# Kernel tuning notes

Measured on AMD Instinct MI355X. Metric: run time of the kernel, lower is better.

Reference implementation:

```python
import math
import jax, jax.numpy as jnp
import numpy as np

D = 1024
NH = 16
DH = D // NH


def setup_inputs() -> dict:
    key = jax.random.key(0)
    k1, k2, k3 = jax.random.split(key, 3)
    x = jax.random.normal(k1, (2, 2048, D), dtype=jnp.float32)
    s = 1.0 / math.sqrt(D)
    W_qkv = jax.random.normal(k2, (D, 3 * D), dtype=jnp.float32) * s
    W_o = jax.random.normal(k3, (D, D), dtype=jnp.float32) * s
    return {"x": x, "W_qkv": W_qkv, "W_o": W_o}


def _rope(q, k, base=10000.0):
    # q, k: [B, H, T, dh]
    half = q.shape[-1] // 2
    freqs = jnp.arange(half, dtype=q.dtype) / half
    theta = 1.0 / base ** freqs                      # [half]
    t = jnp.arange(q.shape[-2], dtype=q.dtype)       # [T]
    ang = t[:, None] * theta[None, :]                # [T, half]
    cos = jnp.cos(ang)[None, None, :, :]
    sin = jnp.sin(ang)[None, None, :, :]

    def rot(x):
        x1, x2 = x[..., :half], x[..., half:]
        return jnp.concatenate([x1 * cos - x2 * sin, x1 * sin + x2 * cos], axis=-1)

    return rot(q), rot(k)


def reference(x, W_qkv, W_o):
    B, T, d = x.shape
    qkv = x @ W_qkv                                   # [B, T, 3D]
    q, k, v = jnp.split(qkv, 3, axis=-1)
    q = q.reshape(B, T, NH, DH).transpose(0, 2, 1, 3)  # [B, H, T, dh]
    k = k.reshape(B, T, NH, DH).transpose(0, 2, 1, 3)
    v = v.reshape(B, T, NH, DH).transpose(0, 2, 1, 3)
    q, k = _rope(q, k)
    att = jnp.einsum('bhtd,bhsd->bhts', q, k) / math.sqrt(DH)  # [B, H, T, T]
    mask = jnp.triu(jnp.full((T, T), -jnp.inf, dtype=att.dtype), 1)
    att = att + mask
    w = jax.nn.softmax(att, axis=-1)
    y = jnp.einsum('bhts,bhsd->bhtd', w, v)           # [B, H, T, dh]
    y = y.transpose(0, 2, 1, 3).reshape(B, T, d)
    return y @ W_o
```

## Files before the change

### kernel.cpp

```cpp
#include <hip/hip_runtime.h>

typedef __bf16 bf16x8 __attribute__((ext_vector_type(8)));
typedef float f32x4 __attribute__((ext_vector_type(4)));
typedef float f32x16 __attribute__((ext_vector_type(16)));

constexpr int SEQ = 2048;
constexpr int DMODEL = 1024;

#define GLL(gp, lp)                                                              \
  __builtin_amdgcn_global_load_lds((const __attribute__((address_space(1))) void*)(gp), \
                                   (__attribute__((address_space(3))) void*)(lp), 16, 0, 0)

__global__ __launch_bounds__(256) void prep_kernel(const float* __restrict__ x,
                                                   const float* __restrict__ Wqkv,
                                                   const float* __restrict__ Wo,
                                                   __bf16* __restrict__ xbf,
                                                   __bf16* __restrict__ WqkvT,
                                                   __bf16* __restrict__ WoT,
                                                   float2* __restrict__ sct) {
  __shared__ __bf16 tile[64][72];
  int blk = blockIdx.x, t = threadIdx.x;

  if (blk < 256) {
    int i = blk * 256 + t;
    int tt = i >> 5, j = i & 31;
    float theta = exp2f(-(float)j * 0.41524101186092953f);
    float s, c;
    __sincosf((float)tt * theta, &s, &c);
    sct[i] = make_float2(c, s);
    return;
  }
  if (blk >= 1280) {
    size_t i = (size_t)(blk - 1280) * 256 + t;
    const float* sp = x + i * 8;
    float4 f0 = *reinterpret_cast<const float4*>(sp);
    float4 f1 = *reinterpret_cast<const float4*>(sp + 4);
    alignas(16) __bf16 tmp[8];
    tmp[0] = (__bf16)f0.x; tmp[1] = (__bf16)f0.y; tmp[2] = (__bf16)f0.z; tmp[3] = (__bf16)f0.w;
    tmp[4] = (__bf16)f1.x; tmp[5] = (__bf16)f1.y; tmp[6] = (__bf16)f1.z; tmp[7] = (__bf16)f1.w;
    *reinterpret_cast<uint4*>(xbf + i * 8) = *reinterpret_cast<const uint4*>(tmp);
    return;
  }
  const float* src;
  __bf16* dst;
  int C, R, c0, r0;
  if (blk < 512) {
    int idx = blk - 256;
    src = Wo; dst = WoT; R = 1024; C = 1024;
    c0 = (idx & 15) * 64; r0 = (idx >> 4) * 64;
  } else {
    int idx = blk - 512;
    src = Wqkv; dst = WqkvT; R = 1024; C = 3072;
    c0 = (idx % 48) * 64; r0 = (idx / 48) * 64;
  }
#pragma unroll
  for (int p = 0; p < 2; ++p) {
    int flat = p * 256 + t;
    int i = flat >> 3;
    int j8 = (flat & 7) * 8;
    const float* sp = &src[(size_t)(r0 + i) * C + c0 + j8];
    float4 f0 = *reinterpret_cast<const float4*>(sp);
    float4 f1 = *reinterpret_cast<const float4*>(sp + 4);
    tile[i][j8 + 0] = (__bf16)f0.x; tile[i][j8 + 1] = (__bf16)f0.y;
    tile[i][j8 + 2] = (__bf16)f0.z; tile[i][j8 + 3] = (__bf16)f0.w;
    tile[i][j8 + 4] = (__bf16)f1.x; tile[i][j8 + 5] = (__bf16)f1.y;
    tile[i][j8 + 6] = (__bf16)f1.z; tile[i][j8 + 7] = (__bf16)f1.w;
  }
  __syncthreads();
#pragma unroll
  for (int p = 0; p < 2; ++p) {
    int flat = p * 256 + t;
    int i = flat >> 3;
    int j8 = (flat & 7) * 8;
    alignas(16) __bf16 tmp[8];
#pragma unroll
    for (int jj = 0; jj < 8; ++jj) tmp[jj] = tile[j8 + jj][i];
    *reinterpret_cast<uint4*>(&dst[(size_t)(c0 + i) * R + r0 + j8]) =
        *reinterpret_cast<const uint4*>(tmp);
  }
}

template <typename CT, int BN, int MODE>
__global__ __launch_bounds__(256) void gemm_bt_lds(const __bf16* __restrict__ A,
                                                   const __bf16* __restrict__ BT,
                                                   CT* __restrict__ C,
                                                   int M, int N, int K, int lda, int ldc,
                                                   const float2* __restrict__ sct,
                                                   __bf16* __restrict__ vt) {
  constexpr int MF = (BN == 128) ? 4 : 2;
  __shared__ __align__(16) __bf16 A_lds[128][64];
  __shared__ __align__(16) __bf16 B_lds[BN][64];
  int tid = threadIdx.x;
  int lane = tid & 63, w = tid >> 6;
  int g = lane >> 4, l15 = lane & 15;
  int wr = (BN == 128) ? (w >> 1) : w;
  int wc = (BN == 128) ? (w & 1) : 0;
  int m0 = blockIdx.x * 128;
  int n0 = blockIdx.y * BN;
  int srow = lane >> 3, scol = (lane & 7) * 8;

  const __bf16* ag = A + (size_t)(m0 + w * 32 + srow) * lda + scol;
  const __bf16* bg = BT + (size_t)(n0 + w * (BN / 4) + srow) * K + scol;

  f32x4 acc[MF][4] = {};

  for (int k0 = 0; k0 < K; k0 += 64) {
    __syncthreads();
#pragma unroll
    for (int i = 0; i < 4; ++i)
      GLL(ag + (size_t)(i * 8) * lda + k0, &A_lds[w * 32 + i * 8][0]);
#pragma unroll
    for (int i = 0; i < BN / 32; ++i)
      GLL(bg + (size_t)(i * 8) * K + k0, &B_lds[w * (BN / 4) + i * 8][0]);
    __syncthreads();
#pragma unroll
    for (int kk = 0; kk < 2; ++kk) {
      bf16x8 a[MF], bb[4];
#pragma unroll
      for (int m = 0; m < MF; ++m)
        a[m] = *reinterpret_cast<const bf16x8*>(&A_lds[wr * (MF * 16) + m * 16 + l15][kk * 32 + g * 8]);
#pragma unroll
      for (int n = 0; n < 4; ++n)
        bb[n] = *reinterpret_cast<const bf16x8*>(&B_lds[wc * 64 + n * 16 + l15][kk * 32 + g * 8]);
#pragma unroll
      for (int m = 0; m < MF; ++m)
#pragma unroll
        for (int n = 0; n < 4; ++n)
          acc[m][n] = __builtin_amdgcn_mfma_f32_16x16x32_bf16(a[m], bb[n], acc[m][n], 0, 0, 0);
    }
  }

  if constexpr (MODE == 3) {
    if (n0 >= 2048) {
      __shared__ __bf16 T_lds[128][72];
      int b = m0 >> 11;
      int s_base = m0 & (SEQ - 1);
#pragma unroll
      for (int half = 0; half < 2; ++half) {
        __syncthreads();
        if (wc == half) {
#pragma unroll
          for (int m = 0; m < MF; ++m)
#pragma unroll
            for (int n = 0; n < 4; ++n)
#pragma unroll
              for (int r = 0; r < 4; ++r)
                T_lds[wr * 64 + m * 16 + 4 * g + r][n * 16 + l15] = (__bf16)acc[m][n][r];
        }
        __syncthreads();
        int head = ((n0 - 2048) >> 6) + half;
        int bh = b * 16 + head;
        int d = tid >> 2;
        int s8 = (tid & 3) * 32;
        __bf16* dst = vt + (size_t)bh * 64 * SEQ + (size_t)d * SEQ + s_base + s8;
#pragma unroll
        for (int j = 0; j < 4; ++j) {
          alignas(16) __bf16 tmp[8];
#pragma unroll
          for (int e = 0; e < 8; ++e) tmp[e] = T_lds[s8 + j * 8 + e][d];
          *reinterpret_cast<uint4*>(dst + j * 8) = *reinterpret_cast<const uint4*>(tmp);
        }
      }
      return;
    }
    bool isq = (n0 < 1024);
    float sc = isq ? 0.18033688011112042f : 1.0f;
#pragma unroll
    for (int m = 0; m < MF; ++m)
#pragma unroll
      for (int r = 0; r < 4; ++r) {
        int row = m0 + wr * (MF * 16) + m * 16 + 4 * g + r;
        int t = row & (SEQ - 1);
#pragma unroll
        for (int n = 0; n < 2; ++n) {
          int j = n * 16 + l15;
          float2 cs = sct[(t << 5) + j];
          float x1 = acc[m][n][r], x2 = acc[m][n + 2][r];
          acc[m][n][r]     = (x1 * cs.x - x2 * cs.y) * sc;
          acc[m][n + 2][r] = (x1 * cs.y + x2 * cs.x) * sc;
        }
      }
  }

#pragma unroll
  for (int m = 0; m < MF; ++m)
#pragma unroll
    for (int n = 0; n < 4; ++n)
#pragma unroll
      for (int r = 0; r < 4; ++r) {
        int row = m0 + wr * (MF * 16) + m * 16 + 4 * g + r;
        int col = n0 + wc * 64 + n * 16 + l15;
        C[(size_t)row * ldc + col] = (CT)acc[m][n][r];
      }
}

__device__ inline uint32_t pkbf(float a, float b) {
  union { __bf16 h[2]; uint32_t u; } z;
  z.h[0] = (__bf16)a; z.h[1] = (__bf16)b;
  return z.u;
}

__device__ inline __bf16* slot_base(int gi, __bf16* qkv, __bf16* xbf, int q_local) {
  if (gi < 1024)
    return qkv + (size_t)(gi * 4 + (q_local >> 4)) * 3072 + 2048 + (q_local & 15) * 64;
  return xbf + (size_t)(gi - 1024) * 4096 + (size_t)q_local * 64;
}

__global__ __launch_bounds__(128, 3) void attn_kernel(__bf16* __restrict__ qkv,
                                                      const __bf16* __restrict__ vt,
                                                      __bf16* __restrict__ xbf,
                                                      float* __restrict__ pml) {
  __shared__ __align__(16) __bf16 K_lds[2][64][64];

  int tid = threadIdx.x;
  int w = tid >> 6, lane = tid & 63;
  int l31 = lane & 31, hi = lane >> 5;
  int bid = blockIdx.x;
  int it = bid >> 5, bh = bid & 31;
  int b = bh >> 4, h = bh & 15;

  int qc = 31 - (it >> 1);
  int half = it & 1;
  int NTf = qc + 1;
  int hs = (NTf + 1) >> 1;
  int kv0 = half ? hs : 0;
  int kv1 = half ? NTf : hs;
  int NT = kv1 - kv0;

  __bf16* qbase = qkv + (size_t)b * SEQ * 3072 + h * 64;
  const __bf16* kbase = qbase + 1024;
  const __bf16* vtb = vt + (size_t)bh * 64 * SEQ;

  int q_g = qc * 64 + w * 32 + l31;

  int r8 = lane >> 3;
  int cxe = 8 * ((lane & 7) ^ r8);

  auto STAGE = [&](int bufv, int t) {
#pragma unroll
    for (int i = 0; i < 4; ++i) {
      int R = w * 32 + i * 8;
      GLL(kbase + (size_t)(t * 64 + R + r8) * 3072 + cxe, &K_lds[bufv][R][0]);
    }
  };

  bf16x8 qf[4];
#pragma unroll
  for (int ds = 0; ds < 4; ++ds)
    qf[ds] = *reinterpret_cast<const bf16x8*>(qbase + (size_t)q_g * 3072 + ds * 16 + 8 * hi);

  f32x16 oacc[2] = {};
  float l_run = 0.f;
  const float MFIX = 8.0f;

  if (NT > 0) STAGE(0, kv0);
  __syncthreads();

  int buf = 0;
  for (int jb = 0; jb < NT; ++jb) {
    int kt_g = kv0 + jb;
    bool pre = (jb + 1 < NT);
    if (pre) STAGE(buf ^ 1, kt_g + 1);

    uint4 vr[8];
#pragma unroll
    for (int dt = 0; dt < 2; ++dt)
#pragma unroll
      for (int ks = 0; ks < 4; ++ks)
        vr[dt * 4 + ks] = *reinterpret_cast<const uint4*>(
            vtb + (size_t)(dt * 32 + l31) * SEQ + kt_g * 64 + ks * 16 + 8 * hi);

    f32x16 sacc[2] = {};
    __builtin_amdgcn_s_setprio(1);
#pragma unroll
    for (int kt = 0; kt < 2; ++kt) {
#pragma unroll
      for (int ds = 0; ds < 4; ++ds) {
        bf16x8 kf = *reinterpret_cast<const bf16x8*>(
            &K_lds[buf][kt * 32 + l31][(ds * 16 + 8 * hi) ^ ((l31 & 7) * 8)]);
        sacc[kt] = __builtin_amdgcn_mfma_f32_32x32x16_bf16(kf, qf[ds], sacc[kt], 0, 0, 0);
      }
    }
    __builtin_amdgcn_s_setprio(0);

    if (kt_g == qc) {
#pragma unroll
      for (int kt = 0; kt < 2; ++kt)
#pragma unroll
        for (int r = 0; r < 16; ++r) {
          int k_g = kt_g * 64 + kt * 32 + (r & 3) + 8 * (r >> 2) + 4 * hi;
          if (k_g > q_g) sacc[kt][r] = -1e30f;
        }
    }

    float s0 = 0.f, s1 = 0.f, s2 = 0.f, s3 = 0.f;
#pragma unroll
    for (int kt = 0; kt < 2; ++kt) {
#pragma unroll
      for (int r = 0; r < 16; r += 4) {
        float p0 = exp2f(sacc[kt][r + 0] - MFIX);
        float p1 = exp2f(sacc[kt][r + 1] - MFIX);
        float p2 = exp2f(sacc[kt][r + 2] - MFIX);
        float p3 = exp2f(sacc[kt][r + 3] - MFIX);
        sacc[kt][r + 0] = p0; sacc[kt][r + 1] = p1;
        sacc[kt][r + 2] = p2; sacc[kt][r + 3] = p3;
        s0 += p0; s1 += p1; s2 += p2; s3 += p3;
      }
    }
    float sum = (s0 + s1) + (s2 + s3);
    sum += __shfl_xor(sum, 32);
    l_run += sum;

    uint4 pa[4];
#pragma unroll
    for (int ks = 0; ks < 4; ++ks) {
      int v0 = 2 * ks, v1 = v0 + 1;
      int t0 = v0 >> 2, rb0 = 4 * (v0 & 3);
      int t1 = v1 >> 2, rb1 = 4 * (v1 & 3);
      uint32_t a01, a23, b01, b23;
      if (t0 == 0) { a01 = pkbf(sacc[0][rb0 + 0], sacc[0][rb0 + 1]);
                     a23 = pkbf(sacc[0][rb0 + 2], sacc[0][rb0 + 3]); }
      else         { a01 = pkbf(sacc[1][rb0 + 0], sacc[1][rb0 + 1]);
                     a23 = pkbf(sacc[1][rb0 + 2], sacc[1][rb0 + 3]); }
      if (t1 == 0) { b01 = pkbf(sacc[0][rb1 + 0], sacc[0][rb1 + 1]);
                     b23 = pkbf(sacc[0][rb1 + 2], sacc[0][rb1 + 3]); }
      else         { b01 = pkbf(sacc[1][rb1 + 0], sacc[1][rb1 + 1]);
                     b23 = pkbf(sacc[1][rb1 + 2], sacc[1][rb1 + 3]); }
      uint32_t t01 = hi ? a01 : b01;
      uint32_t t23 = hi ? a23 : b23;
      uint32_t r01 = __shfl_xor(t01, 32);
      uint32_t r23 = __shfl_xor(t23, 32);
      uint32_t k01 = hi ? b01 : a01;
      uint32_t k23 = hi ? b23 : a23;
      pa[ks].x = hi ? r01 : k01;
      pa[ks].y = hi ? r23 : k23;
      pa[ks].z = hi ? k01 : r01;
      pa[ks].w = hi ? k23 : r23;
    }

    __builtin_amdgcn_s_setprio(1);
#pragma unroll
    for (int dt = 0; dt < 2; ++dt) {
#pragma unroll
      for (int ks = 0; ks < 4; ++ks) {
        oacc[dt] = __builtin_amdgcn_mfma_f32_32x32x16_bf16(
            *reinterpret_cast<const bf16x8*>(&vr[dt * 4 + ks]),
            *reinterpret_cast<const bf16x8*>(&pa[ks]), oacc[dt], 0, 0, 0);
      }
    }
    __builtin_amdgcn_s_setprio(0);

    if (pre) {
      asm volatile("s_waitcnt vmcnt(0)" ::: "memory");
      __syncthreads();
    }
    buf ^= 1;
  }

  int gi = ((31 - qc) * 2 + half) * 32 + bh;
  int q_local = w * 32 + l31;
  __bf16* pobase = slot_base(gi, qkv, xbf, q_local);
#pragma unroll
  for (int dt = 0; dt < 2; ++dt)
#pragma unroll
    for (int u = 0; u < 4; ++u) {
      int d0 = dt * 32 + 8 * u + 4 * hi;
      alignas(8) __bf16 tmp[4];
#pragma unroll
      for (int m = 0; m < 4; ++m) tmp[m] = (__bf16)oacc[dt][4 * u + m];
      *reinterpret_cast<uint2*>(pobase + d0) = *reinterpret_cast<const uint2*>(tmp);
    }
  if (hi == 0) pml[gi * 128 + q_local] = l_run;
}

__global__ __launch_bounds__(128) void combine_kernel(__bf16* __restrict__ qkv,
                                                      __bf16* __restrict__ xbf,
                                                      const float* __restrict__ pml) {
  int bid = blockIdx.x;
  int qc = 31 - (bid >> 5), bh = bid & 31;
  int b = bh >> 4, h = bh & 15;
  int t = threadIdx.x;
  int q = t >> 1, dh = (t & 1) * 32;

  int g0 = ((31 - qc) * 2 + 0) * 32 + bh;
  int g1 = g0 + 32;
  float l0 = pml[g0 * 128 + q];
  float l1 = pml[g1 * 128 + q];
  float inv = 1.0f / (l0 + l1);

  const __bf16* p0 = slot_base(g0, qkv, xbf, q) + dh;
  const __bf16* p1 = slot_base(g1, qkv, xbf, q) + dh;
  __bf16* yq = qkv + (size_t)(b * SEQ + qc * 64 + q) * 3072 + h * 64 + dh;

#pragma unroll
  for (int c = 0; c < 4; ++c) {
    uint4 ua = *reinterpret_cast<const uint4*>(p0 + c * 8);
    uint4 ub = *reinterpret_cast<const uint4*>(p1 + c * 8);
    const __bf16* va = reinterpret_cast<const __bf16*>(&ua);
    const __bf16* vb = reinterpret_cast<const __bf16*>(&ub);
    alignas(16) __bf16 outv[8];
#pragma unroll
    for (int j = 0; j < 8; ++j)
      outv[j] = (__bf16)((((float)va[j]) + ((float)vb[j])) * inv);
    *reinterpret_cast<uint4*>(yq + c * 8) = *reinterpret_cast<const uint4*>(outv);
  }
}

extern "C" void kernel_launch(void* const* d_in, const int* in_sizes, int n_in,
                              void* d_out, int out_size, void* d_ws, size_t ws_size,
                              hipStream_t stream) {
  const float* x = (const float*)d_in[0];
  const float* Wqkv = (const float*)d_in[1];
  const float* Wo = (const float*)d_in[2];
  float* out = (float*)d_out;

  __bf16* ws = (__bf16*)d_ws;
  __bf16* WqkvT = ws;
  __bf16* WoT = WqkvT + (size_t)3072 * 1024;
  __bf16* qkv = WoT + (size_t)1024 * 1024;
  __bf16* xbf = qkv + (size_t)4096 * 3072;
  __bf16* vtb = xbf + (size_t)4096 * 1024;
  float* pml = (float*)(vtb + (size_t)32 * 64 * SEQ);
  float2* sct = (float2*)(pml + 2048 * 128);

  prep_kernel<<<3328, 256, 0, stream>>>(x, Wqkv, Wo, xbf, WqkvT, WoT, sct);

  gemm_bt_lds<__bf16, 128, 3><<<dim3(32, 24), 256, 0, stream>>>(
      xbf, WqkvT, qkv, 4096, 3072, 1024, 1024, 3072, sct, vtb);

  attn_kernel<<<2048, 128, 0, stream>>>(qkv, vtb, xbf, pml);

  combine_kernel<<<1024, 128, 0, stream>>>(qkv, xbf, pml);

  gemm_bt_lds<float, 64, 0><<<dim3(32, 16), 256, 0, stream>>>(
      qkv, WoT, out, 4096, 1024, 1024, 3072, 1024, sct, nullptr);
}
```

Baseline: 139.1 us.

## Use 512-thread GEMM blocks with smaller per-wave tiles and shared LDS buffer

Both GEMMs now launch 8 waves per block instead of 4, and each wave computes a 32xBN/2 sub-tile, so it holds fewer accumulators. The A/B LDS buffers are merged, and the V-transpose staging buffer reuses that storage instead of allocating its own. The goal is more waves in flight to hide global-to-LDS load latency, at the cost of more synchronisation per k-step and fewer MFMAs per LDS fragment load.

```diff
diff --git a/kernel.cpp b/kernel.cpp
--- a/kernel.cpp
+++ b/kernel.cpp
@@ -81,58 +81,62 @@
 }
 
 template <typename CT, int BN, int MODE>
-__global__ __launch_bounds__(256) void gemm_bt_lds(const __bf16* __restrict__ A,
-                                                   const __bf16* __restrict__ BT,
-                                                   CT* __restrict__ C,
-                                                   int M, int N, int K, int lda, int ldc,
-                                                   const float2* __restrict__ sct,
-                                                   __bf16* __restrict__ vt) {
-  constexpr int MF = (BN == 128) ? 4 : 2;
-  __shared__ __align__(16) __bf16 A_lds[128][64];
-  __shared__ __align__(16) __bf16 B_lds[BN][64];
+__global__ __launch_bounds__(512, 6) void gemm_bt_lds(const __bf16* __restrict__ A,
+                                                      const __bf16* __restrict__ BT,
+                                                      CT* __restrict__ C,
+                                                      int M, int N, int K, int lda, int ldc,
+                                                      const float2* __restrict__ sct,
+                                                      __bf16* __restrict__ vt) {
+  constexpr int NF = BN / 32;
+  __shared__ __align__(16) __bf16 AB_lds[128 + BN][64];
+  __bf16 (*A_lds)[64] = &AB_lds[0];
+  __bf16 (*B_lds)[64] = &AB_lds[128];
+
   int tid = threadIdx.x;
   int lane = tid & 63, w = tid >> 6;
   int g = lane >> 4, l15 = lane & 15;
-  int wr = (BN == 128) ? (w >> 1) : w;
-  int wc = (BN == 128) ? (w & 1) : 0;
+  int wr = w & 3;
+  int wc = w >> 2;
   int m0 = blockIdx.x * 128;
   int n0 = blockIdx.y * BN;
-  int srow = lane >> 3, scol = (lane & 7) * 8;
-
-  const __bf16* ag = A + (size_t)(m0 + w * 32 + srow) * lda + scol;
-  const __bf16* bg = BT + (size_t)(n0 + w * (BN / 4) + srow) * K + scol;
-
-  f32x4 acc[MF][4] = {};
+  int r8 = lane >> 3, scol = (lane & 7) * 8;
+
+  const __bf16* ag = A + (size_t)(m0 + w * 16 + r8) * lda + scol;
+  const __bf16* bg = BT + (size_t)(n0 + w * (BN / 8) + r8) * K + scol;
+
+  f32x4 acc[2][NF] = {};
 
   for (int k0 = 0; k0 < K; k0 += 64) {
     __syncthreads();
-#pragma unroll
-    for (int i = 0; i < 4; ++i)
-      GLL(ag + (size_t)(i * 8) * lda + k0, &A_lds[w * 32 + i * 8][0]);
-#pragma unroll
-    for (int i = 0; i < BN / 32; ++i)
-      GLL(bg + (size_t)(i * 8) * K + k0, &B_lds[w * (BN / 4) + i * 8][0]);
+    GLL(ag + k0, &A_lds[w * 16][0]);
+    GLL(ag + (size_t)8 * lda + k0, &A_lds[w * 16 + 8][0]);
+    if constexpr (BN == 128) {
+      GLL(bg + k0, &B_lds[w * 16][0]);
+      GLL(bg + (size_t)8 * K + k0, &B_lds[w * 16 + 8][0]);
+    } else {
+      GLL(bg + k0, &B_lds[w * 8][0]);
+    }
     __syncthreads();
 #pragma unroll
     for (int kk = 0; kk < 2; ++kk) {
-      bf16x8 a[MF], bb[4];
-#pragma unroll
-      for (int m = 0; m < MF; ++m)
-        a[m] = *reinterpret_cast<const bf16x8*>(&A_lds[wr * (MF * 16) + m * 16 + l15][kk * 32 + g * 8]);
-#pragma unroll
-      for (int n = 0; n < 4; ++n)
-        bb[n] = *reinterpret_cast<const bf16x8*>(&B_lds[wc * 64 + n * 16 + l15][kk * 32 + g * 8]);
-#pragma unroll
-      for (int m = 0; m < MF; ++m)
-#pragma unroll
-        for (int n = 0; n < 4; ++n)
+      bf16x8 a[2], bb[NF];
+#pragma unroll
+      for (int m = 0; m < 2; ++m)
+        a[m] = *reinterpret_cast<const bf16x8*>(&A_lds[wr * 32 + m * 16 + l15][kk * 32 + g * 8]);
+#pragma unroll
+      for (int n = 0; n < NF; ++n)
+        bb[n] = *reinterpret_cast<const bf16x8*>(&B_lds[wc * (BN / 2) + n * 16 + l15][kk * 32 + g * 8]);
+#pragma unroll
+      for (int m = 0; m < 2; ++m)
+#pragma unroll
+        for (int n = 0; n < NF; ++n)
           acc[m][n] = __builtin_amdgcn_mfma_f32_16x16x32_bf16(a[m], bb[n], acc[m][n], 0, 0, 0);
     }
   }
 
   if constexpr (MODE == 3) {
     if (n0 >= 2048) {
-      __shared__ __bf16 T_lds[128][72];
+      __bf16 (*T_lds)[72] = reinterpret_cast<__bf16(*)[72]>(&AB_lds[0][0]);
       int b = m0 >> 11;
       int s_base = m0 & (SEQ - 1);
 #pragma unroll
@@ -140,21 +144,21 @@
         __syncthreads();
         if (wc == half) {
 #pragma unroll
-          for (int m = 0; m < MF; ++m)
-#pragma unroll
-            for (int n = 0; n < 4; ++n)
+          for (int m = 0; m < 2; ++m)
+#pragma unroll
+            for (int n = 0; n < NF; ++n)
 #pragma unroll
               for (int r = 0; r < 4; ++r)
-                T_lds[wr * 64 + m * 16 + 4 * g + r][n * 16 + l15] = (__bf16)acc[m][n][r];
+                T_lds[wr * 32 + m * 16 + 4 * g + r][n * 16 + l15] = (__bf16)acc[m][n][r];
         }
         __syncthreads();
         int head = ((n0 - 2048) >> 6) + half;
         int bh = b * 16 + head;
-        int d = tid >> 2;
-        int s8 = (tid & 3) * 32;
+        int d = tid >> 3;
+        int s8 = (tid & 7) * 16;
         __bf16* dst = vt + (size_t)bh * 64 * SEQ + (size_t)d * SEQ + s_base + s8;
 #pragma unroll
-        for (int j = 0; j < 4; ++j) {
+        for (int j = 0; j < 2; ++j) {
           alignas(16) __bf16 tmp[8];
 #pragma unroll
           for (int e = 0; e < 8; ++e) tmp[e] = T_lds[s8 + j * 8 + e][d];
@@ -166,10 +170,10 @@
     bool isq = (n0 < 1024);
     float sc = isq ? 0.18033688011112042f : 1.0f;
 #pragma unroll
-    for (int m = 0; m < MF; ++m)
+    for (int m = 0; m < 2; ++m)
 #pragma unroll
       for (int r = 0; r < 4; ++r) {
-        int row = m0 + wr * (MF * 16) + m * 16 + 4 * g + r;
+        int row = m0 + wr * 32 + m * 16 + 4 * g + r;
         int t = row & (SEQ - 1);
 #pragma unroll
         for (int n = 0; n < 2; ++n) {
@@ -183,13 +187,13 @@
   }
 
 #pragma unroll
-  for (int m = 0; m < MF; ++m)
-#pragma unroll
-    for (int n = 0; n < 4; ++n)
+  for (int m = 0; m < 2; ++m)
+#pragma unroll
+    for (int n = 0; n < NF; ++n)
 #pragma unroll
       for (int r = 0; r < 4; ++r) {
-        int row = m0 + wr * (MF * 16) + m * 16 + 4 * g + r;
-        int col = n0 + wc * 64 + n * 16 + l15;
+        int row = m0 + wr * 32 + m * 16 + 4 * g + r;
+        int col = n0 + wc * (BN / 2) + n * 16 + l15;
         C[(size_t)row * ldc + col] = (CT)acc[m][n][r];
       }
 }
@@ -425,13 +429,13 @@
 
   prep_kernel<<<3328, 256, 0, stream>>>(x, Wqkv, Wo, xbf, WqkvT, WoT, sct);
 
-  gemm_bt_lds<__bf16, 128, 3><<<dim3(32, 24), 256, 0, stream>>>(
+  gemm_bt_lds<__bf16, 128, 3><<<dim3(32, 24), 512, 0, stream>>>(
       xbf, WqkvT, qkv, 4096, 3072, 1024, 1024, 3072, sct, vtb);
 
   attn_kernel<<<2048, 128, 0, stream>>>(qkv, vtb, xbf, pml);
 
   combine_kernel<<<1024, 128, 0, stream>>>(qkv, xbf, pml);
 
-  gemm_bt_lds<float, 64, 0><<<dim3(32, 16), 256, 0, stream>>>(
+  gemm_bt_lds<float, 64, 0><<<dim3(32, 16), 512, 0, stream>>>(
       qkv, WoT, out, 4096, 1024, 1024, 3072, 1024, sct, nullptr);
 }
```

New measurement: 132.5 us, median of 2. 4.8% less time.
